# Performance work log

Measured on AMD Instinct MI355X. Metric: run time of the kernel, lower is better.

The kernel has to match this reference:

```python
import jax, jax.numpy as jnp
import numpy as np

ALPHA = 0.2       # LeakyReLU negative slope
MASK_FILL = 1e-15 # value placed at non-edges before softmax (as in the original)
OUT_DIM = 64


def setup_inputs() -> dict:
    key = jax.random.key(0)
    k1, k2, k3, k4 = jax.random.split(key, 4)
    N, IN_DIM, D = 8192, 256, OUT_DIM
    h = jax.random.normal(k1, (N, IN_DIM), dtype=jnp.float32)
    # dense 0/1 adjacency (float, used only via A > 0)
    A = jax.random.randint(k2, (N, N), 0, 2).astype(jnp.float32)
    W = jax.random.normal(k3, (IN_DIM, D), dtype=jnp.float32) * (1.0 / np.sqrt(IN_DIM))
    a = jax.random.normal(k4, (2 * D,), dtype=jnp.float32) * (1.0 / np.sqrt(2 * D))
    return {"h": h, "A": A, "W": W, "a": a}


def reference(h, A, W, a):
    D = OUT_DIM
    Wh = h @ W                                   # [N, D]
    # attn([Wh_i || Wh_j]) == Wh_i . a[:D] + Wh_j . a[D:]  -- fused, avoids [N,N,2D]
    s_src = Wh @ a[:D]                           # [N]
    s_dst = Wh @ a[D:]                           # [N]
    e = jax.nn.leaky_relu(s_src[:, None] + s_dst[None, :], negative_slope=ALPHA)  # [N, N]
    attention = jnp.where(A > 0, e, MASK_FILL)
    attention = jax.nn.softmax(attention, axis=1)
    h_prime = attention @ Wh                     # [N, D]
    return jax.nn.elu(h_prime)                   # concat=True branch
```

## Files before the change

kernel.cpp:

```cpp
#include <hip/hip_runtime.h>
#include <hip/hip_bf16.h>

#define GAT_N 8192
#define GAT_K 256
#define GAT_D 64
#define GAT_ALPHA 0.2f
#define GAT_FILL 1e-15f

typedef float f32x4 __attribute__((ext_vector_type(4)));
typedef short bf16x8 __attribute__((ext_vector_type(8)));

static __device__ __forceinline__ unsigned f2bf_u(float x) {
  unsigned u = __float_as_uint(x);
  u += 0x7FFFu + ((u >> 16) & 1u);
  return u >> 16;
}

__global__ __launch_bounds__(256) void k_prep(const float* __restrict__ h,
                                              const float* __restrict__ W,
                                              const float* __restrict__ av,
                                              float* __restrict__ s_src,
                                              float* __restrict__ s_dst,
                                              short* __restrict__ WhT,
                                              float* __restrict__ bmax) {
  __shared__ short T[4][64][8];
  __shared__ float wmLds[4];
  const int tid = threadIdx.x;
  const int wv = tid >> 6, lane = tid & 63;
  const int r0 = blockIdx.x * 32 + wv * 8;

  float acc[8], acc2[8];
#pragma unroll
  for (int r = 0; r < 8; ++r) { acc[r] = 0.f; acc2[r] = 0.f; }

  for (int kc = 0; kc < GAT_K; kc += 32) {
    float Wreg[32];
#pragma unroll
    for (int e = 0; e < 32; ++e) Wreg[e] = W[(size_t)(kc + e) * GAT_D + lane];
#pragma unroll
    for (int r = 0; r < 8; ++r) {
      const f32x4* h4 = (const f32x4*)(h + (size_t)(r0 + r) * GAT_K + kc);
#pragma unroll
      for (int q = 0; q < 8; ++q) {
        f32x4 hv = h4[q];
        acc[r] += hv[0] * Wreg[4 * q + 0];
        acc2[r] += hv[1] * Wreg[4 * q + 1];
        acc[r] += hv[2] * Wreg[4 * q + 2];
        acc2[r] += hv[3] * Wreg[4 * q + 3];
      }
    }
  }

  const float a_s = av[lane];
  const float a_d = av[64 + lane];
  float wmax = -3.0e38f;
#pragma unroll
  for (int r = 0; r < 8; ++r) {
    const float accf = acc[r] + acc2[r];
    T[wv][lane][r] = (short)f2bf_u(accf);
    float vs = accf * a_s, vd = accf * a_d;
#pragma unroll
    for (int off = 32; off > 0; off >>= 1) {
      vs += __shfl_xor(vs, off);
      vd += __shfl_xor(vd, off);
    }
    if (lane == 0) { s_src[r0 + r] = vs; s_dst[r0 + r] = vd; }
    wmax = fmaxf(wmax, vd);
  }
  bf16x8 vt = *(const bf16x8*)&T[wv][lane][0];
  *(bf16x8*)(WhT + (size_t)lane * GAT_N + r0) = vt;

  if (lane == 0) wmLds[wv] = wmax;
  __syncthreads();
  if (tid == 0) {
    bmax[blockIdx.x] = fmaxf(fmaxf(wmLds[0], wmLds[1]), fmaxf(wmLds[2], wmLds[3]));
  }
}

#define BM 16

__global__ __launch_bounds__(256, 2) void k_attn(
    const float* __restrict__ A,
    const float* __restrict__ s_src,
    const float* __restrict__ s_dst,
    const short* __restrict__ WhT,
    const float* __restrict__ bmax,
    float* __restrict__ out) {
  __shared__ char smem[16640];

  const int tid = threadIdx.x;
  const int wv = tid >> 6, lane = tid & 63;
  const int hi = lane >> 5, l5 = lane & 31;
  const int rsub = lane & 15, kg = lane >> 4;
  const int i0 = blockIdx.x * BM;
  const int wvbase = wv << 12;

  float bm = fmaxf(fmaxf(bmax[lane], bmax[lane + 64]),
                   fmaxf(bmax[lane + 128], bmax[lane + 192]));
#pragma unroll
  for (int off = 32; off > 0; off >>= 1) bm = fmaxf(bm, __shfl_xor(bm, off));
  const float tmax = bm;

  float F1_[8], F2_[8], ns_[8], cc_[8];
#pragma unroll
  for (int s = 0; s < 8; ++s) {
    const int row = 2 * s + hi;
    float sc = s_src[i0 + row];
    float x0 = sc + tmax;
    float m = fmaxf(fmaxf(x0, GAT_ALPHA * x0), GAT_FILL);
    F1_[s] = __expf(sc - m);
    F2_[s] = __expf(GAT_ALPHA * sc - m);
    ns_[s] = -sc;
    cc_[s] = __expf(GAT_FILL - m);
  }

  bf16x8 ones;
#pragma unroll
  for (int e = 0; e < 8; ++e) ones[e] = (short)0x3F80;

  f32x4 acc0 = {0.f, 0.f, 0.f, 0.f};
  f32x4 acc1 = {0.f, 0.f, 0.f, 0.f};
  f32x4 acc2 = {0.f, 0.f, 0.f, 0.f};
  f32x4 acc3 = {0.f, 0.f, 0.f, 0.f};
  f32x4 accl = {0.f, 0.f, 0.f, 0.f};

  const int colbase = wv * 128;
  const float* Abase = A + (size_t)(i0 + hi) * GAT_N + colbase + l5 * 4;
  const short* pb0 = WhT + (size_t)(0 * 16 + rsub) * GAT_N + colbase + (kg << 3);
  const short* pb1 = WhT + (size_t)(1 * 16 + rsub) * GAT_N + colbase + (kg << 3);
  const short* pb2 = WhT + (size_t)(2 * 16 + rsub) * GAT_N + colbase + (kg << 3);
  const short* pb3 = WhT + (size_t)(3 * 16 + rsub) * GAT_N + colbase + (kg << 3);
  const float* tbase = s_dst + colbase + l5 * 4;

  f32x4 Ar[8];
#pragma unroll
  for (int s = 0; s < 8; ++s)
    Ar[s] = *(const f32x4*)(Abase + (size_t)(2 * s) * GAT_N);
  bf16x8 bq0[4], bq1[4], bq2[4], bq3[4];
#pragma unroll
  for (int kq = 0; kq < 4; ++kq) {
    bq0[kq] = *(const bf16x8*)(pb0 + (kq << 5));
    bq1[kq] = *(const bf16x8*)(pb1 + (kq << 5));
    bq2[kq] = *(const bf16x8*)(pb2 + (kq << 5));
    bq3[kq] = *(const bf16x8*)(pb3 + (kq << 5));
  }
  f32x4 tcur = *(const f32x4*)tbase;

  for (int c = 0; c < 16; ++c) {
    const int jc = c * 512;
    const int jn = (c < 15) ? jc + 512 : jc;

    f32x4 tnxt = *(const f32x4*)(tbase + jn);

    f32x4 E1, E2;
#pragma unroll
    for (int e = 0; e < 4; ++e) {
      E1[e] = __expf(tcur[e]);
      E2[e] = __expf(GAT_ALPHA * tcur[e]);
    }

#pragma unroll
    for (int s = 0; s < 8; ++s) {
      f32x4 av = Ar[s];
      Ar[s] = *(const f32x4*)(Abase + (size_t)(2 * s) * GAT_N + jn);
      float p[4];
#pragma unroll
      for (int e = 0; e < 4; ++e) {
        float m1 = E1[e] * F1_[s];
        float m2 = E2[e] * F2_[s];
        float psel = (tcur[e] >= ns_[s]) ? m1 : m2;
        p[e] = (av[e] > 0.f) ? psel : cc_[s];
      }
      __hip_bfloat162 pa = __float22bfloat162_rn(float2{p[0], p[1]});
      __hip_bfloat162 pb = __float22bfloat162_rn(float2{p[2], p[3]});
      uint2 w;
      __builtin_memcpy(&w.x, &pa, 4);
      __builtin_memcpy(&w.y, &pb, 4);
      const int row = 2 * s + hi;
      *(uint2*)(&smem[wvbase + (row << 8) + ((l5 << 3) ^ ((row & 7) << 4))]) = w;
    }

#pragma unroll
    for (int kq = 0; kq < 4; ++kq) {
      const int raddr =
          wvbase + (rsub << 8) + (((kq << 6) | (kg << 4)) ^ ((rsub & 7) << 4));
      bf16x8 af = *(const bf16x8*)(&smem[raddr]);
      acc0 = __builtin_amdgcn_mfma_f32_16x16x32_bf16(af, bq0[kq], acc0, 0, 0, 0);
      acc1 = __builtin_amdgcn_mfma_f32_16x16x32_bf16(af, bq1[kq], acc1, 0, 0, 0);
      acc2 = __builtin_amdgcn_mfma_f32_16x16x32_bf16(af, bq2[kq], acc2, 0, 0, 0);
      acc3 = __builtin_amdgcn_mfma_f32_16x16x32_bf16(af, bq3[kq], acc3, 0, 0, 0);
      accl = __builtin_amdgcn_mfma_f32_16x16x32_bf16(af, ones, accl, 0, 0, 0);
      bq0[kq] = *(const bf16x8*)(pb0 + jn + (kq << 5));
      bq1[kq] = *(const bf16x8*)(pb1 + jn + (kq << 5));
      bq2[kq] = *(const bf16x8*)(pb2 + jn + (kq << 5));
      bq3[kq] = *(const bf16x8*)(pb3 + jn + (kq << 5));
    }
    tcur = tnxt;
  }

  __syncthreads();

  float* lds_o = (float*)smem;
  float* lds_l = (float*)(smem + 16384);
#pragma unroll
  for (int r = 0; r < 4; ++r) {
    const int orow = kg * 4 + r;
    lds_o[wv * 1024 + orow * 64 + 0 * 16 + rsub] = acc0[r];
    lds_o[wv * 1024 + orow * 64 + 1 * 16 + rsub] = acc1[r];
    lds_o[wv * 1024 + orow * 64 + 2 * 16 + rsub] = acc2[r];
    lds_o[wv * 1024 + orow * 64 + 3 * 16 + rsub] = acc3[r];
    if (rsub == 0) lds_l[wv * 16 + orow] = accl[r];
  }
  __syncthreads();

  for (int idx = tid; idx < BM * GAT_D; idx += 256) {
    const int r = idx >> 6, col = idx & 63;
    float o = 0.f, ll = 0.f;
#pragma unroll
    for (int w = 0; w < 4; ++w) {
      o += lds_o[w * 1024 + r * 64 + col];
      ll += lds_l[w * 16 + r];
    }
    float val = o / ll;
    out[(size_t)(i0 + r) * GAT_D + col] = (val > 0.f) ? val : (__expf(val) - 1.f);
  }
}

extern "C" void kernel_launch(void* const* d_in, const int* in_sizes, int n_in,
                              void* d_out, int out_size, void* d_ws, size_t ws_size,
                              hipStream_t stream) {
  const float* h = (const float*)d_in[0];
  const float* A = (const float*)d_in[1];
  const float* W = (const float*)d_in[2];
  const float* a = (const float*)d_in[3];
  float* out = (float*)d_out;

  const size_t need = 69632 + (size_t)GAT_D * GAT_N * 2;
  if (ws_size < need) return;
  float* bmax = (float*)d_ws;
  float* s_src = (float*)((char*)d_ws + 4096);
  float* s_dst = (float*)((char*)d_ws + 36864);
  short* WhT = (short*)((char*)d_ws + 69632);

  k_prep<<<dim3(256), dim3(256), 0, stream>>>(h, W, a, s_src, s_dst, WhT, bmax);
  k_attn<<<dim3(GAT_N / BM), dim3(256), 0, stream>>>(A, s_src, s_dst, WhT, bmax, out);
}
```

Before: 125.7 us.

## Tile WhT by column chunk, rotate chunk order per block, deepen A prefetch

Measured after the change: 138.2 us. 9.9% more time.

```diff
diff --git a/kernel.cpp b/kernel.cpp
--- a/kernel.cpp
+++ b/kernel.cpp
@@ -68,7 +68,7 @@
     wmax = fmaxf(wmax, vd);
   }
   bf16x8 vt = *(const bf16x8*)&T[wv][lane][0];
-  *(bf16x8*)(WhT + (size_t)lane * GAT_N + r0) = vt;
+  *(bf16x8*)(WhT + (size_t)(r0 >> 9) * 32768 + (size_t)lane * 512 + (r0 & 511)) = vt;
 
   if (lane == 0) wmLds[wv] = wmax;
   __syncthreads();
@@ -86,7 +86,7 @@
     const short* __restrict__ WhT,
     const float* __restrict__ bmax,
     float* __restrict__ out) {
-  __shared__ char smem[16640];
+  __shared__ char smem[16896];
 
   const int tid = threadIdx.x;
   const int wv = tid >> 6, lane = tid & 63;
@@ -94,6 +94,9 @@
   const int rsub = lane & 15, kg = lane >> 4;
   const int i0 = blockIdx.x * BM;
   const int wvbase = wv << 12;
+  const int rot = blockIdx.x & 15;
+
+  float* scon = (float*)(smem + 16640);
 
   float bm = fmaxf(fmaxf(bmax[lane], bmax[lane + 64]),
                    fmaxf(bmax[lane + 128], bmax[lane + 192]));
@@ -101,18 +104,16 @@
   for (int off = 32; off > 0; off >>= 1) bm = fmaxf(bm, __shfl_xor(bm, off));
   const float tmax = bm;
 
-  float F1_[8], F2_[8], ns_[8], cc_[8];
-#pragma unroll
-  for (int s = 0; s < 8; ++s) {
-    const int row = 2 * s + hi;
-    float sc = s_src[i0 + row];
+  if (tid < BM) {
+    float sc = s_src[i0 + tid];
     float x0 = sc + tmax;
     float m = fmaxf(fmaxf(x0, GAT_ALPHA * x0), GAT_FILL);
-    F1_[s] = __expf(sc - m);
-    F2_[s] = __expf(GAT_ALPHA * sc - m);
-    ns_[s] = -sc;
-    cc_[s] = __expf(GAT_FILL - m);
-  }
+    scon[tid] = __expf(sc - m);
+    scon[16 + tid] = __expf(GAT_ALPHA * sc - m);
+    scon[32 + tid] = -sc;
+    scon[48 + tid] = __expf(GAT_FILL - m);
+  }
+  __syncthreads();
 
   bf16x8 ones;
 #pragma unroll
@@ -124,33 +125,37 @@
   f32x4 acc3 = {0.f, 0.f, 0.f, 0.f};
   f32x4 accl = {0.f, 0.f, 0.f, 0.f};
 
-  const int colbase = wv * 128;
-  const float* Abase = A + (size_t)(i0 + hi) * GAT_N + colbase + l5 * 4;
-  const short* pb0 = WhT + (size_t)(0 * 16 + rsub) * GAT_N + colbase + (kg << 3);
-  const short* pb1 = WhT + (size_t)(1 * 16 + rsub) * GAT_N + colbase + (kg << 3);
-  const short* pb2 = WhT + (size_t)(2 * 16 + rsub) * GAT_N + colbase + (kg << 3);
-  const short* pb3 = WhT + (size_t)(3 * 16 + rsub) * GAT_N + colbase + (kg << 3);
-  const float* tbase = s_dst + colbase + l5 * 4;
-
-  f32x4 Ar[8];
-#pragma unroll
-  for (int s = 0; s < 8; ++s)
-    Ar[s] = *(const f32x4*)(Abase + (size_t)(2 * s) * GAT_N);
+  const float* Abase = A + (size_t)(i0 + hi) * GAT_N + wv * 128 + l5 * 4;
+  const short* pB0 = WhT + (size_t)(0 * 16 + rsub) * 512 + wv * 128 + (kg << 3);
+  const short* pB1 = WhT + (size_t)(1 * 16 + rsub) * 512 + wv * 128 + (kg << 3);
+  const short* pB2 = WhT + (size_t)(2 * 16 + rsub) * 512 + wv * 128 + (kg << 3);
+  const short* pB3 = WhT + (size_t)(3 * 16 + rsub) * 512 + wv * 128 + (kg << 3);
+  const float* tbase = s_dst + wv * 128 + l5 * 4;
+
+  f32x4 ArA[8], ArB[8];
   bf16x8 bq0[4], bq1[4], bq2[4], bq3[4];
-#pragma unroll
-  for (int kq = 0; kq < 4; ++kq) {
-    bq0[kq] = *(const bf16x8*)(pb0 + (kq << 5));
-    bq1[kq] = *(const bf16x8*)(pb1 + (kq << 5));
-    bq2[kq] = *(const bf16x8*)(pb2 + (kq << 5));
-    bq3[kq] = *(const bf16x8*)(pb3 + (kq << 5));
-  }
-  f32x4 tcur = *(const f32x4*)tbase;
-
-  for (int c = 0; c < 16; ++c) {
-    const int jc = c * 512;
-    const int jn = (c < 15) ? jc + 512 : jc;
-
-    f32x4 tnxt = *(const f32x4*)(tbase + jn);
+  f32x4 tcur;
+  {
+    const int cc0 = rot, cc1 = (rot + 1) & 15;
+#pragma unroll
+    for (int s = 0; s < 8; ++s) {
+      ArA[s] = *(const f32x4*)(Abase + (size_t)(2 * s) * GAT_N + cc0 * 512);
+      ArB[s] = *(const f32x4*)(Abase + (size_t)(2 * s) * GAT_N + cc1 * 512);
+    }
+#pragma unroll
+    for (int kq = 0; kq < 4; ++kq) {
+      bq0[kq] = *(const bf16x8*)(pB0 + cc0 * 32768 + (kq << 5));
+      bq1[kq] = *(const bf16x8*)(pB1 + cc0 * 32768 + (kq << 5));
+      bq2[kq] = *(const bf16x8*)(pB2 + cc0 * 32768 + (kq << 5));
+      bq3[kq] = *(const bf16x8*)(pB3 + cc0 * 32768 + (kq << 5));
+    }
+    tcur = *(const f32x4*)(tbase + cc0 * 512);
+  }
+
+  auto chunk_body = [&](int c, f32x4 (&Ar)[8]) {
+    const int cn1 = (c + 1 + rot) & 15;
+    const int cn2 = (c + 2 + rot) & 15;
+    f32x4 tnxt = *(const f32x4*)(tbase + cn1 * 512);
 
     f32x4 E1, E2;
 #pragma unroll
@@ -162,21 +167,23 @@
 #pragma unroll
     for (int s = 0; s < 8; ++s) {
       f32x4 av = Ar[s];
-      Ar[s] = *(const f32x4*)(Abase + (size_t)(2 * s) * GAT_N + jn);
+      Ar[s] = *(const f32x4*)(Abase + (size_t)(2 * s) * GAT_N + cn2 * 512);
+      const int row = 2 * s + hi;
+      const float F1 = scon[row], F2 = scon[16 + row];
+      const float negs = scon[32 + row], cv = scon[48 + row];
       float p[4];
 #pragma unroll
       for (int e = 0; e < 4; ++e) {
-        float m1 = E1[e] * F1_[s];
-        float m2 = E2[e] * F2_[s];
-        float psel = (tcur[e] >= ns_[s]) ? m1 : m2;
-        p[e] = (av[e] > 0.f) ? psel : cc_[s];
+        float m1 = E1[e] * F1;
+        float m2 = E2[e] * F2;
+        float psel = (tcur[e] >= negs) ? m1 : m2;
+        p[e] = (av[e] > 0.f) ? psel : cv;
       }
       __hip_bfloat162 pa = __float22bfloat162_rn(float2{p[0], p[1]});
       __hip_bfloat162 pb = __float22bfloat162_rn(float2{p[2], p[3]});
       uint2 w;
       __builtin_memcpy(&w.x, &pa, 4);
       __builtin_memcpy(&w.y, &pb, 4);
-      const int row = 2 * s + hi;
       *(uint2*)(&smem[wvbase + (row << 8) + ((l5 << 3) ^ ((row & 7) << 4))]) = w;
     }
 
@@ -190,12 +197,17 @@
       acc2 = __builtin_amdgcn_mfma_f32_16x16x32_bf16(af, bq2[kq], acc2, 0, 0, 0);
       acc3 = __builtin_amdgcn_mfma_f32_16x16x32_bf16(af, bq3[kq], acc3, 0, 0, 0);
       accl = __builtin_amdgcn_mfma_f32_16x16x32_bf16(af, ones, accl, 0, 0, 0);
-      bq0[kq] = *(const bf16x8*)(pb0 + jn + (kq << 5));
-      bq1[kq] = *(const bf16x8*)(pb1 + jn + (kq << 5));
-      bq2[kq] = *(const bf16x8*)(pb2 + jn + (kq << 5));
-      bq3[kq] = *(const bf16x8*)(pb3 + jn + (kq << 5));
+      bq0[kq] = *(const bf16x8*)(pB0 + cn1 * 32768 + (kq << 5));
+      bq1[kq] = *(const bf16x8*)(pB1 + cn1 * 32768 + (kq << 5));
+      bq2[kq] = *(const bf16x8*)(pB2 + cn1 * 32768 + (kq << 5));
+      bq3[kq] = *(const bf16x8*)(pB3 + cn1 * 32768 + (kq << 5));
     }
     tcur = tnxt;
+  };
+
+  for (int cp = 0; cp < 8; ++cp) {
+    chunk_body(2 * cp, ArA);
+    chunk_body(2 * cp + 1, ArB);
   }
 
   __syncthreads();
```

## Stream adjacency tiles into LDS asynchronously with 512-thread blocks and chunk rotation

Applied to the files above, without the earlier changes.

Result: slower. 135.5 us (+7.8%).

```diff
diff --git a/kernel.cpp b/kernel.cpp
--- a/kernel.cpp
+++ b/kernel.cpp
@@ -9,6 +9,9 @@
 
 typedef float f32x4 __attribute__((ext_vector_type(4)));
 typedef short bf16x8 __attribute__((ext_vector_type(8)));
+
+typedef __attribute__((address_space(3))) unsigned char lds_byte;
+typedef __attribute__((address_space(1))) const unsigned char glb_byte;
 
 static __device__ __forceinline__ unsigned f2bf_u(float x) {
   unsigned u = __float_as_uint(x);
@@ -68,7 +71,7 @@
     wmax = fmaxf(wmax, vd);
   }
   bf16x8 vt = *(const bf16x8*)&T[wv][lane][0];
-  *(bf16x8*)(WhT + (size_t)lane * GAT_N + r0) = vt;
+  *(bf16x8*)(WhT + (size_t)(r0 >> 9) * 32768 + (size_t)lane * 512 + (r0 & 511)) = vt;
 
   if (lane == 0) wmLds[wv] = wmax;
   __syncthreads();
@@ -79,21 +82,23 @@
 
 #define BM 16
 
-__global__ __launch_bounds__(256, 2) void k_attn(
+__global__ __launch_bounds__(512, 4) void k_attn(
     const float* __restrict__ A,
     const float* __restrict__ s_src,
     const float* __restrict__ s_dst,
     const short* __restrict__ WhT,
     const float* __restrict__ bmax,
     float* __restrict__ out) {
-  __shared__ char smem[16640];
+  __shared__ char smem[81920];
 
   const int tid = threadIdx.x;
   const int wv = tid >> 6, lane = tid & 63;
-  const int hi = lane >> 5, l5 = lane & 31;
+  const int sub = lane & 15, rg = lane >> 4;
   const int rsub = lane & 15, kg = lane >> 4;
   const int i0 = blockIdx.x * BM;
-  const int wvbase = wv << 12;
+  const int rot = blockIdx.x & 15;
+  const int abase = wv * 8192;
+  const int tbase = 65536 + wv * 2048;
 
   float bm = fmaxf(fmaxf(bmax[lane], bmax[lane + 64]),
                    fmaxf(bmax[lane + 128], bmax[lane + 192]));
@@ -101,10 +106,10 @@
   for (int off = 32; off > 0; off >>= 1) bm = fmaxf(bm, __shfl_xor(bm, off));
   const float tmax = bm;
 
-  float F1_[8], F2_[8], ns_[8], cc_[8];
-#pragma unroll
-  for (int s = 0; s < 8; ++s) {
-    const int row = 2 * s + hi;
+  float F1_[4], F2_[4], ns_[4], cc_[4];
+#pragma unroll
+  for (int s = 0; s < 4; ++s) {
+    const int row = 4 * s + rg;
     float sc = s_src[i0 + row];
     float x0 = sc + tmax;
     float m = fmaxf(fmaxf(x0, GAT_ALPHA * x0), GAT_FILL);
@@ -124,51 +129,49 @@
   f32x4 acc3 = {0.f, 0.f, 0.f, 0.f};
   f32x4 accl = {0.f, 0.f, 0.f, 0.f};
 
-  const int colbase = wv * 128;
-  const float* Abase = A + (size_t)(i0 + hi) * GAT_N + colbase + l5 * 4;
-  const short* pb0 = WhT + (size_t)(0 * 16 + rsub) * GAT_N + colbase + (kg << 3);
-  const short* pb1 = WhT + (size_t)(1 * 16 + rsub) * GAT_N + colbase + (kg << 3);
-  const short* pb2 = WhT + (size_t)(2 * 16 + rsub) * GAT_N + colbase + (kg << 3);
-  const short* pb3 = WhT + (size_t)(3 * 16 + rsub) * GAT_N + colbase + (kg << 3);
-  const float* tbase = s_dst + colbase + l5 * 4;
-
-  f32x4 Ar[8];
-#pragma unroll
-  for (int s = 0; s < 8; ++s)
-    Ar[s] = *(const f32x4*)(Abase + (size_t)(2 * s) * GAT_N);
-  bf16x8 bq0[4], bq1[4], bq2[4], bq3[4];
-#pragma unroll
-  for (int kq = 0; kq < 4; ++kq) {
-    bq0[kq] = *(const bf16x8*)(pb0 + (kq << 5));
-    bq1[kq] = *(const bf16x8*)(pb1 + (kq << 5));
-    bq2[kq] = *(const bf16x8*)(pb2 + (kq << 5));
-    bq3[kq] = *(const bf16x8*)(pb3 + (kq << 5));
-  }
-  f32x4 tcur = *(const f32x4*)tbase;
-
-  for (int c = 0; c < 16; ++c) {
-    const int jc = c * 512;
-    const int jn = (c < 15) ? jc + 512 : jc;
-
-    f32x4 tnxt = *(const f32x4*)(tbase + jn);
+  const float* Ab = A + (size_t)(i0 + rg) * GAT_N + wv * 64 + sub * 4;
+  const short* pB0 = WhT + (size_t)(0 * 16 + rsub) * 512 + wv * 64 + (kg << 3);
+  const short* pB1 = WhT + (size_t)(1 * 16 + rsub) * 512 + wv * 64 + (kg << 3);
+  const short* pB2 = WhT + (size_t)(2 * 16 + rsub) * 512 + wv * 64 + (kg << 3);
+  const short* pB3 = WhT + (size_t)(3 * 16 + rsub) * 512 + wv * 64 + (kg << 3);
+  const float* tb = s_dst + wv * 64 + sub * 4;
+
+  auto issue = [&](int cg, int bufoff) {
+#pragma unroll
+    for (int i = 0; i < 4; ++i) {
+      const float* g = Ab + (size_t)(4 * i) * GAT_N + cg * 512;
+      __builtin_amdgcn_global_load_lds(
+          (glb_byte*)g, (lds_byte*)&smem[abase + bufoff + i * 1024], 16, 0, 0);
+    }
+  };
+
+  issue(rot, 0);
+
+  auto body = [&](int c, int bufR, int bufW) {
+    const int cg = (c + rot) & 15;
+    const int cn = (c + 1 + rot) & 15;
+    const f32x4 t = *(const f32x4*)(tb + cg * 512);
+    issue(cn, bufW);
+    asm volatile("s_waitcnt vmcnt(4)" ::: "memory");
+    __builtin_amdgcn_sched_barrier(0);
 
     f32x4 E1, E2;
 #pragma unroll
     for (int e = 0; e < 4; ++e) {
-      E1[e] = __expf(tcur[e]);
-      E2[e] = __expf(GAT_ALPHA * tcur[e]);
-    }
-
-#pragma unroll
-    for (int s = 0; s < 8; ++s) {
-      f32x4 av = Ar[s];
-      Ar[s] = *(const f32x4*)(Abase + (size_t)(2 * s) * GAT_N + jn);
+      E1[e] = __expf(t[e]);
+      E2[e] = __expf(GAT_ALPHA * t[e]);
+    }
+
+#pragma unroll
+    for (int s = 0; s < 4; ++s) {
+      const f32x4 av =
+          *(const f32x4*)(&smem[abase + bufR + s * 1024 + lane * 16]);
       float p[4];
 #pragma unroll
       for (int e = 0; e < 4; ++e) {
         float m1 = E1[e] * F1_[s];
         float m2 = E2[e] * F2_[s];
-        float psel = (tcur[e] >= ns_[s]) ? m1 : m2;
+        float psel = (t[e] >= ns_[s]) ? m1 : m2;
         p[e] = (av[e] > 0.f) ? psel : cc_[s];
       }
       __hip_bfloat162 pa = __float22bfloat162_rn(float2{p[0], p[1]});
@@ -176,32 +179,37 @@
       uint2 w;
       __builtin_memcpy(&w.x, &pa, 4);
       __builtin_memcpy(&w.y, &pb, 4);
-      const int row = 2 * s + hi;
-      *(uint2*)(&smem[wvbase + (row << 8) + ((l5 << 3) ^ ((row & 7) << 4))]) = w;
-    }
-
-#pragma unroll
-    for (int kq = 0; kq < 4; ++kq) {
+      const int row = 4 * s + rg;
+      *(uint2*)(&smem[tbase + (row << 7) + ((sub << 3) ^ ((row & 7) << 4))]) = w;
+    }
+
+#pragma unroll
+    for (int kq = 0; kq < 2; ++kq) {
       const int raddr =
-          wvbase + (rsub << 8) + (((kq << 6) | (kg << 4)) ^ ((rsub & 7) << 4));
+          tbase + (rsub << 7) + (((kq << 6) | (kg << 4)) ^ ((rsub & 7) << 4));
       bf16x8 af = *(const bf16x8*)(&smem[raddr]);
-      acc0 = __builtin_amdgcn_mfma_f32_16x16x32_bf16(af, bq0[kq], acc0, 0, 0, 0);
-      acc1 = __builtin_amdgcn_mfma_f32_16x16x32_bf16(af, bq1[kq], acc1, 0, 0, 0);
-      acc2 = __builtin_amdgcn_mfma_f32_16x16x32_bf16(af, bq2[kq], acc2, 0, 0, 0);
-      acc3 = __builtin_amdgcn_mfma_f32_16x16x32_bf16(af, bq3[kq], acc3, 0, 0, 0);
+      const int boff = cg * 32768 + (kq << 5);
+      bf16x8 b0 = *(const bf16x8*)(pB0 + boff);
+      bf16x8 b1 = *(const bf16x8*)(pB1 + boff);
+      bf16x8 b2 = *(const bf16x8*)(pB2 + boff);
+      bf16x8 b3 = *(const bf16x8*)(pB3 + boff);
+      acc0 = __builtin_amdgcn_mfma_f32_16x16x32_bf16(af, b0, acc0, 0, 0, 0);
+      acc1 = __builtin_amdgcn_mfma_f32_16x16x32_bf16(af, b1, acc1, 0, 0, 0);
+      acc2 = __builtin_amdgcn_mfma_f32_16x16x32_bf16(af, b2, acc2, 0, 0, 0);
+      acc3 = __builtin_amdgcn_mfma_f32_16x16x32_bf16(af, b3, acc3, 0, 0, 0);
       accl = __builtin_amdgcn_mfma_f32_16x16x32_bf16(af, ones, accl, 0, 0, 0);
-      bq0[kq] = *(const bf16x8*)(pb0 + jn + (kq << 5));
-      bq1[kq] = *(const bf16x8*)(pb1 + jn + (kq << 5));
-      bq2[kq] = *(const bf16x8*)(pb2 + jn + (kq << 5));
-      bq3[kq] = *(const bf16x8*)(pb3 + jn + (kq << 5));
-    }
-    tcur = tnxt;
+    }
+  };
+
+  for (int cp = 0; cp < 8; ++cp) {
+    body(2 * cp, 0, 4096);
+    body(2 * cp + 1, 4096, 0);
   }
 
   __syncthreads();
 
   float* lds_o = (float*)smem;
-  float* lds_l = (float*)(smem + 16384);
+  float* lds_l = (float*)(smem + 32768);
 #pragma unroll
   for (int r = 0; r < 4; ++r) {
     const int orow = kg * 4 + r;
@@ -213,11 +221,11 @@
   }
   __syncthreads();
 
-  for (int idx = tid; idx < BM * GAT_D; idx += 256) {
+  for (int idx = tid; idx < BM * GAT_D; idx += 512) {
     const int r = idx >> 6, col = idx & 63;
     float o = 0.f, ll = 0.f;
 #pragma unroll
-    for (int w = 0; w < 4; ++w) {
+    for (int w = 0; w < 8; ++w) {
       o += lds_o[w * 1024 + r * 64 + col];
       ll += lds_l[w * 16 + r];
     }
@@ -243,5 +251,5 @@
   short* WhT = (short*)((char*)d_ws + 69632);
 
   k_prep<<<dim3(256), dim3(256), 0, stream>>>(h, W, a, s_src, s_dst, WhT, bmax);
-  k_attn<<<dim3(GAT_N / BM), dim3(256), 0, stream>>>(A, s_src, s_dst, WhT, bmax, out);
-}
+  k_attn<<<dim3(GAT_N / BM), dim3(512), 0, stream>>>(A, s_src, s_dst, WhT, bmax, out);
+}
```
